# Kernel optimization log

Hardware: AMD Instinct MI355X
Metric: run time of the kernel (lower is better)

The kernel has to match this reference:

```python
import jax, jax.numpy as jnp
import numpy as np

NUM_HEADS = 8
NUM_GROUPS = 32
EPS = 1e-5


def group_norm(x, scale, bias):
    # x: (b, c, t)
    b, c, t = x.shape
    xg = x.reshape(b, NUM_GROUPS, c // NUM_GROUPS, t)
    mean = xg.mean(axis=(2, 3), keepdims=True)
    var = xg.var(axis=(2, 3), keepdims=True)
    xn = ((xg - mean) * jax.lax.rsqrt(var + EPS)).reshape(b, c, t)
    return xn * scale[None, :, None] + bias[None, :, None]


def setup_inputs() -> dict:
    key = jax.random.key(0)
    ks = jax.random.split(key, 3)
    b, c, h, w = 16, 512, 32, 32
    x = jax.random.normal(ks[0], (b, c, h, w), dtype=jnp.float32)
    gn_scale = jnp.ones((c,), jnp.float32)
    gn_bias = jnp.zeros((c,), jnp.float32)
    w_qkv = jax.random.normal(ks[1], (3 * c, c), jnp.float32) * (c ** -0.5)
    b_qkv = jnp.zeros((3 * c,), jnp.float32)
    w_proj = jax.random.normal(ks[2], (c, c), jnp.float32) * (c ** -0.5)
    b_proj = jnp.zeros((c,), jnp.float32)
    return {"x": x, "gn_scale": gn_scale, "gn_bias": gn_bias,
            "w_qkv": w_qkv, "b_qkv": b_qkv, "w_proj": w_proj, "b_proj": b_proj}


def reference(x, gn_scale, gn_bias, w_qkv, b_qkv, w_proj, b_proj):
    b, c, h, w = x.shape
    t = h * w
    xf = x.reshape(b, c, t)
    xn = group_norm(xf, gn_scale, gn_bias)
    # 1x1 conv1d == channel matmul: (b, 3c, t)
    qkv = jnp.einsum('oc,bct->bot', w_qkv, xn) + b_qkv[None, :, None]
    dh = c // NUM_HEADS
    qkv = qkv.reshape(b * NUM_HEADS, 3 * dh, t)
    q, k, v = jnp.split(qkv, 3, axis=1)  # each (b*H, dh, t)
    scale = dh ** -0.25
    logits = jnp.einsum('bct,bcs->bts', q * scale, k * scale)
    weight = jax.nn.softmax(logits.astype(jnp.float32), axis=-1).astype(logits.dtype)
    attn = jnp.einsum('bts,bcs->bct', weight, v)  # (b*H, dh, t)
    attn = attn.reshape(b, c, t)
    out = jnp.einsum('oc,bct->bot', w_proj, attn) + b_proj[None, :, None]
    return (xf + out).reshape(b, c, h, w)
```

## Files before the change

kernel.cpp:

```cpp
#include <hip/hip_runtime.h>
#include <hip/hip_bf16.h>

typedef __hip_bfloat16 bf16;
typedef __attribute__((ext_vector_type(8))) short short8;
typedef __attribute__((ext_vector_type(4))) short short4v;
typedef __attribute__((ext_vector_type(4))) float float4v;
typedef __attribute__((ext_vector_type(16))) float f32x16;
typedef __attribute__((ext_vector_type(4))) int int4v;

__device__ __forceinline__ float b2f(bf16 v) { return __bfloat162float(v); }
__device__ __forceinline__ bf16  f2b(float v) { return __float2bfloat16(v); }
__device__ __forceinline__ short f2s(float v) { bf16 h = f2b(v); return *reinterpret_cast<short*>(&h); }
__device__ __forceinline__ float s2f(short s) { bf16 h; *reinterpret_cast<short*>(&h) = s; return b2f(h); }
__device__ __forceinline__ short8 ld8(const bf16* p) { return *(const short8*)p; }

__device__ __forceinline__ float ldin(const void* p, size_t i, int f32) {
  return f32 ? ((const float*)p)[i] : b2f(((const bf16*)p)[i]);
}

__device__ __forceinline__ float4v mfma16(short8 a, short8 b, float4v c) {
  return __builtin_amdgcn_mfma_f32_16x16x32_bf16(a, b, c, 0, 0, 0);
}
__device__ __forceinline__ f32x16 mfma32(short8 a, short8 b, f32x16 c) {
  return __builtin_amdgcn_mfma_f32_32x32x16_bf16(a, b, c, 0, 0, 0);
}
__device__ __forceinline__ int cvtpk(float a, float b) {
  int r; asm("v_cvt_pk_bf16_f32 %0, %1, %2" : "=v"(r) : "v"(a), "v"(b)); return r;
}
__device__ __forceinline__ void plswap(int& x, int& y) {
  asm("v_permlane32_swap_b32 %0, %1" : "+v"(x), "+v"(y));
}

__device__ __forceinline__ void gload16(const void* g, void* l) {
  __builtin_amdgcn_global_load_lds((__attribute__((address_space(1))) void*)(void*)g,
                                   (__attribute__((address_space(3))) void*)l, 16, 0, 0);
}

#define K2SCALE 0.18033688011112042f
#define TSTRIDE 72

__global__ __launch_bounds__(256) void detect_kernel(const unsigned short* __restrict__ x,
                                                     int* __restrict__ flag) {
  __shared__ int h;
  if (threadIdx.x == 0) h = 0;
  __syncthreads();
  int local = 0;
  for (int i = threadIdx.x; i < 8192; i += 256)
    if ((x[i] & 0x7F80u) == 0x7F80u) local = 1;
  if (local) atomicOr(&h, 1);
  __syncthreads();
  if (threadIdx.x == 0) *flag = h;
}

__global__ __launch_bounds__(256) void pre_kernel(const void* __restrict__ s1, bf16* __restrict__ d1,
                                                  const void* __restrict__ s2, bf16* __restrict__ d2,
                                                  const void* __restrict__ s3, bf16* __restrict__ d3,
                                                  const void* __restrict__ s4, bf16* __restrict__ d4,
                                                  const void* __restrict__ x,
                                                  float2* __restrict__ stats,
                                                  const int* __restrict__ flagp) {
  const int f32 = *flagp;
  const int blk = blockIdx.x;
  const int tid = threadIdx.x;
  __shared__ float rs[4], rss[4];

  if (blk < 1027) {
    const void* src; bf16* dst; int base, n;
    if (blk < 768)       { src = s1; dst = d1; base = blk;        n = 786432; }
    else if (blk < 1024) { src = s2; dst = d2; base = blk - 768;  n = 262144; }
    else if (blk < 1026) { src = s3; dst = d3; base = blk - 1024; n = 1536;   }
    else                 { src = s4; dst = d4; base = 0;          n = 512;    }
    int i0 = (base * 256 + tid) * 4;
#pragma unroll
    for (int j = 0; j < 4; j++) {
      int i = i0 + j;
      if (i < n) dst[i] = f2b(ldin(src, i, f32));
    }
    return;
  }

  const int bg = blk - 1027;
  const int GSZ = 16 * 1024;
  const size_t base = (size_t)bg * GSZ;

  float s = 0.f, ss = 0.f;
  if (f32) {
    const float4v* xp = (const float4v*)((const float*)x + base) + tid;
#pragma unroll
    for (int i = 0; i < 16; i++) {
      float4v v = xp[i * 256];
#pragma unroll
      for (int j = 0; j < 4; j++) { s += v[j]; ss += v[j] * v[j]; }
    }
  } else {
    const short8* xp = (const short8*)((const bf16*)x + base) + tid;
#pragma unroll
    for (int i = 0; i < 8; i++) {
      short8 v = xp[i * 256];
#pragma unroll
      for (int j = 0; j < 8; j++) { float f = s2f(v[j]); s += f; ss += f * f; }
    }
  }
  for (int off = 32; off > 0; off >>= 1) {
    s  += __shfl_down(s, off);
    ss += __shfl_down(ss, off);
  }
  const int wave = tid >> 6, lane = tid & 63;
  if (lane == 0) { rs[wave] = s; rss[wave] = ss; }
  __syncthreads();
  if (tid == 0) {
    s  = rs[0] + rs[1] + rs[2] + rs[3];
    ss = rss[0] + rss[1] + rss[2] + rss[3];
    const float mean = s * (1.f / GSZ);
    const float var  = ss * (1.f / GSZ) - mean * mean;
    stats[bg] = make_float2(mean, rsqrtf(var + 1e-5f));
  }
}

__global__ __launch_bounds__(256) void gn_apply_kernel(const void* __restrict__ x,
                                                       const void* __restrict__ gsc,
                                                       const void* __restrict__ gbi,
                                                       const float2* __restrict__ stats,
                                                       bf16* __restrict__ xn,
                                                       const int* __restrict__ flagp) {
  const int f32 = *flagp;
  const int b = blockIdx.y;
  const int t0 = blockIdx.x * 64;
  const int cs = blockIdx.z * 128;
  const int tid = threadIdx.x;

  __shared__ float Aa[128], Bb[128];
  __shared__ short T[64][130];

  if (tid < 128) {
    const int c = cs + tid;
    const float2 st = stats[b * 32 + (c >> 4)];
    const float sc = ldin(gsc, c, f32), bi = ldin(gbi, c, f32);
    Aa[tid] = st.y * sc;
    Bb[tid] = bi - st.x * st.y * sc;
  }
  __syncthreads();

  const int row = tid >> 4;
  const int t4 = (tid & 15) * 4;
  if (f32) {
    const float* xb = (const float*)x + ((size_t)(b * 512 + cs)) * 1024 + t0 + t4;
#pragma unroll
    for (int st = 0; st < 8; st++) {
      const int c = row + st * 16;
      const float4v v = *(const float4v*)(xb + (size_t)c * 1024);
      const float aa = Aa[c], bb = Bb[c];
#pragma unroll
      for (int j = 0; j < 4; j++) T[t4 + j][c] = f2s(v[j] * aa + bb);
    }
  } else {
    const bf16* xb = (const bf16*)x + ((size_t)(b * 512 + cs)) * 1024 + t0 + t4;
#pragma unroll
    for (int st = 0; st < 8; st++) {
      const int c = row + st * 16;
      const short4v v = *(const short4v*)(xb + (size_t)c * 1024);
      const float aa = Aa[c], bb = Bb[c];
#pragma unroll
      for (int j = 0; j < 4; j++) T[t4 + j][c] = f2s(s2f(v[j]) * aa + bb);
    }
  }
  __syncthreads();

  const int cc = (tid & 63) * 2, tr = tid >> 6;
#pragma unroll
  for (int i = 0; i < 16; i++) {
    const int t2 = tr + i * 4;
    const int v = *(const int*)&T[t2][cc];
    *(int*)&xn[((size_t)(b * 1024 + t0 + t2)) * 512 + cs + cc] = v;
  }
}

__global__ __launch_bounds__(256) void qkv_kernel(const bf16* __restrict__ Wb,
                                                  const bf16* __restrict__ biasb,
                                                  const bf16* __restrict__ xn,
                                                  bf16* __restrict__ Qt,
                                                  bf16* __restrict__ Kt,
                                                  bf16* __restrict__ Vb) {
  const int bat = blockIdx.z;
  const int M0 = blockIdx.y * 128;
  const int N0 = blockIdx.x * 128;
  __shared__ short smem[18432];

  const int tid = threadIdx.x;
  const int w = tid >> 6, lane = tid & 63;
  const int col = lane & 15, g = lane >> 4;
  const int wm = (w & 1) * 64, wn = (w >> 1) * 64;

  float4v acc[4][4];
#pragma unroll
  for (int i = 0; i < 4; i++)
#pragma unroll
    for (int j = 0; j < 4; j++) acc[i][j] = (float4v)(0.f);

  int srco[2], dstb[2];
#pragma unroll
  for (int i = 0; i < 2; i++) {
    const int Gb = i * 256 + w * 64;
    dstb[i] = Gb * 8;
    const int G = Gb + lane;
    srco[i] = (G >> 2) * 512 + (G & 3) * 8;
  }
  const bf16* Ab  = Wb + (size_t)M0 * 512;
  const bf16* Bb2 = xn + ((size_t)bat * 1024 + N0) * 512;

#pragma unroll
  for (int i = 0; i < 2; i++) {
    gload16(Ab + srco[i],  &smem[dstb[i]]);
    gload16(Bb2 + srco[i], &smem[4096 + dstb[i]]);
  }
  __syncthreads();

  for (int it = 0; it < 16; ++it) {
    const int pb = it & 1;
    if (it < 15) {
      const int kn = it * 32 + 32;
      const int nb = (1 - pb) * 8192;
#pragma unroll
      for (int i = 0; i < 2; i++) {
        gload16(Ab + kn + srco[i],  &smem[nb + dstb[i]]);
        gload16(Bb2 + kn + srco[i], &smem[nb + 4096 + dstb[i]]);
      }
    }
    const short* Ap = &smem[pb * 8192];
    const short* Bp = Ap + 4096;
    short8 af[4], bf4[4];
#pragma unroll
    for (int mt = 0; mt < 4; mt++) af[mt] = *(const short8*)&Ap[(wm + mt * 16 + col) * 32 + g * 8];
#pragma unroll
    for (int nt = 0; nt < 4; nt++) bf4[nt] = *(const short8*)&Bp[(wn + nt * 16 + col) * 32 + g * 8];
#pragma unroll
    for (int mt = 0; mt < 4; mt++)
#pragma unroll
      for (int nt = 0; nt < 4; nt++) acc[mt][nt] = mfma16(af[mt], bf4[nt], acc[mt][nt]);
    __syncthreads();
  }

  const int sec = (M0 + wm) >> 6;
  const int h = sec / 3, kind = sec % 3;
  const size_t bh = (size_t)bat * 8 + h;
  const float qs = (kind == 0) ? K2SCALE : 1.f;
  short* Tw = smem + w * 4608;

  float bv[4][4];
#pragma unroll
  for (int mt = 0; mt < 4; mt++)
#pragma unroll
    for (int r = 0; r < 4; r++) bv[mt][r] = b2f(biasb[M0 + wm + mt * 16 + g * 4 + r]);

  if (kind == 2) {
#pragma unroll
    for (int mt = 0; mt < 4; mt++)
#pragma unroll
      for (int nt = 0; nt < 4; nt++)
#pragma unroll
        for (int r = 0; r < 4; r++) {
          const int lo = mt * 16 + g * 4 + r;
          const int lt = nt * 16 + col;
          Tw[lo * TSTRIDE + lt] = f2s(acc[mt][nt][r] + bv[mt][r]);
        }
#pragma unroll
    for (int j = 0; j < 8; j++) {
      const int lo = j * 8 + (lane >> 3);
      const int gr = lane & 7;
      short8 v = *(const short8*)&Tw[lo * TSTRIDE + gr * 8];
      *(short8*)(Vb + (bh * 64 + lo) * 1024 + N0 + wn + gr * 8) = v;
    }
  } else {
#pragma unroll
    for (int mt = 0; mt < 4; mt++)
#pragma unroll
      for (int nt = 0; nt < 4; nt++) {
        short4v pk;
#pragma unroll
        for (int r = 0; r < 4; r++) pk[r] = f2s((acc[mt][nt][r] + bv[mt][r]) * qs);
        *(short4v*)&Tw[(nt * 16 + col) * TSTRIDE + mt * 16 + g * 4] = pk;
      }
    bf16* dst = (kind == 0) ? Qt : Kt;
#pragma unroll
    for (int j = 0; j < 8; j++) {
      const int tl = j * 8 + (lane >> 3), c8 = (lane & 7) * 8;
      short8 v = *(const short8*)&Tw[tl * TSTRIDE + c8];
      *(short8*)(dst + (bh * 1024 + N0 + wn + tl) * 64 + c8) = v;
    }
  }
}

__global__ __launch_bounds__(256, 2) void attn_kernel(const bf16* __restrict__ Qt,
                                                      const bf16* __restrict__ Kt,
                                                      const bf16* __restrict__ Vb,
                                                      bf16* __restrict__ xattn) {
  const int bh = blockIdx.x;
  const int t0 = blockIdx.y * 256;
  const int b = bh >> 3, h = bh & 7;
  const int tid = threadIdx.x;
  const int w = tid >> 6, lane = tid & 63;
  const int qv = lane & 31, hh = lane >> 5;
  const int q0 = t0 + w * 64;

  __shared__ short Ks[8192];
  __shared__ short Vs[8192];

  const bf16* kbase = Kt + (size_t)bh * 65536;
  const bf16* vbase = Vb + (size_t)bh * 65536;

  int ksrc[2], vsrc[2];
  const int ldst0 = w * 1024, ldst1 = w * 1024 + 512;
#pragma unroll
  for (int i = 0; i < 2; i++) {
    const int G = w * 128 + i * 64 + lane;
    const int a = G >> 8, ks = (G >> 6) & 3, qvs = (G >> 1) & 31, hhs = G & 1;
    const int co = (ks * 2 + hhs) * 8;
    ksrc[i] = (a * 32 + qvs) * 64 + co;
    vsrc[i] = (a * 32 + qvs) * 1024 + co;
  }
  const int rb = (qv * 2 + hh) * 8;

  short8 qb[2][4];
#pragma unroll
  for (int qt = 0; qt < 2; qt++)
#pragma unroll
    for (int ks = 0; ks < 4; ks++)
      qb[qt][ks] = ld8(Qt + ((size_t)bh * 1024 + q0 + qt * 32 + qv) * 64 + ks * 16 + hh * 8);

  f32x16 O[2][2];
#pragma unroll
  for (int qt = 0; qt < 2; qt++)
#pragma unroll
    for (int o = 0; o < 2; o++) O[qt][o] = (f32x16)(0.f);
  float l[2] = {0.f, 0.f};
  short8 pa[2][4];

  gload16(kbase + ksrc[0], &Ks[ldst0]);
  gload16(kbase + ksrc[1], &Ks[ldst1]);
  gload16(vbase + vsrc[0], &Vs[ldst0]);
  gload16(vbase + vsrc[1], &Vs[ldst1]);
  __syncthreads();

#define SMAX(S, qt, a)                                                          \
  {                                                                             \
    _Pragma("unroll")                                                           \
    for (int j = 0; j < 16; j++) S[j] = __builtin_amdgcn_exp2f(S[j]);           \
    l[qt] += (((S[0] + S[1]) + (S[2] + S[3])) + ((S[4] + S[5]) + (S[6] + S[7])))\
       + (((S[8] + S[9]) + (S[10] + S[11])) + ((S[12] + S[13]) + (S[14] + S[15]))); \
    _Pragma("unroll")                                                           \
    for (int kp = 0; kp < 2; kp++) {                                            \
      int X  = cvtpk(S[8 * kp + 0], S[8 * kp + 1]);                             \
      int Y  = cvtpk(S[8 * kp + 4], S[8 * kp + 5]);                             \
      int X2 = cvtpk(S[8 * kp + 2], S[8 * kp + 3]);                             \
      int Y2 = cvtpk(S[8 * kp + 6], S[8 * kp + 7]);                             \
      plswap(X, Y);                                                             \
      plswap(X2, Y2);                                                           \
      const int4v wv = {X, X2, Y, Y2};                                          \
      pa[qt][(a) * 2 + kp] = __builtin_bit_cast(short8, wv);                    \
    }                                                                           \
  }

#pragma unroll 2
  for (int it = 0; it < 16; ++it) {
    const int cur = (it & 1) * 4096;
    const int nxt = 4096 - cur;
    if (it < 15) {
      gload16(kbase + (it + 1) * 4096 + ksrc[0], &Ks[nxt + ldst0]);
      gload16(kbase + (it + 1) * 4096 + ksrc[1], &Ks[nxt + ldst1]);
      gload16(vbase + (it + 1) * 64 + vsrc[0],   &Vs[nxt + ldst0]);
      gload16(vbase + (it + 1) * 64 + vsrc[1],   &Vs[nxt + ldst1]);
    }
#pragma unroll
    for (int a = 0; a < 2; a++) {
      short8 kf[4];
#pragma unroll
      for (int ks = 0; ks < 4; ks++)
        kf[ks] = *(const short8*)&Ks[cur + (a * 4 + ks) * 512 + rb];
#pragma unroll
      for (int qt = 0; qt < 2; qt++) {
        f32x16 S = (f32x16)(0.f);
#pragma unroll
        for (int ks = 0; ks < 4; ks++) S = mfma32(kf[ks], qb[qt][ks], S);
        SMAX(S, qt, a);
      }
    }
#pragma unroll
    for (int o = 0; o < 2; o++) {
      short8 vf[4];
#pragma unroll
      for (int ks = 0; ks < 4; ks++)
        vf[ks] = *(const short8*)&Vs[cur + (o * 4 + ks) * 512 + rb];
#pragma unroll
      for (int qt = 0; qt < 2; qt++)
#pragma unroll
        for (int ks = 0; ks < 4; ks++)
          O[qt][o] = mfma32(pa[qt][ks], vf[ks], O[qt][o]);
    }
    __syncthreads();
  }
#undef SMAX

#pragma unroll
  for (int qt = 0; qt < 2; qt++) {
    float lt = l[qt] + __shfl_xor(l[qt], 32);
    const float inv = 1.f / lt;
    float* lf = (float*)Ks + w * 64 + qt * 32;
    lf[qv] = inv;

    bf16* ob = xattn + ((size_t)b * 1024 + q0 + qt * 32 + 4 * hh) * 512 + h * 64 + qv;
#pragma unroll
    for (int r = 0; r < 16; r++) {
      const int qoff = (r & 3) + 8 * (r >> 2);
      const float iv = lf[qoff + 4 * hh];
      ob[(size_t)qoff * 512]      = f2b(O[qt][0][r] * iv);
      ob[(size_t)qoff * 512 + 32] = f2b(O[qt][1][r] * iv);
    }
  }
}

__global__ __launch_bounds__(256) void proj_kernel(const bf16* __restrict__ Wp,
                                                   const bf16* __restrict__ biasb,
                                                   const bf16* __restrict__ xattn,
                                                   const void* __restrict__ res,
                                                   void* __restrict__ out,
                                                   const int* __restrict__ flagp) {
  const int f32 = *flagp;
  const int bat = blockIdx.z;
  const int M0 = blockIdx.y * 128;
  const int N0 = blockIdx.x * 128;
  __shared__ short smem[18432];

  const int tid = threadIdx.x;
  const int w = tid >> 6, lane = tid & 63;
  const int col = lane & 15, g = lane >> 4;
  const int wm = (w & 1) * 64, wn = (w >> 1) * 64;

  float4v acc[4][4];
#pragma unroll
  for (int i = 0; i < 4; i++)
#pragma unroll
    for (int j = 0; j < 4; j++) acc[i][j] = (float4v)(0.f);

  int srco[2], dstb[2];
#pragma unroll
  for (int i = 0; i < 2; i++) {
    const int Gb = i * 256 + w * 64;
    dstb[i] = Gb * 8;
    const int G = Gb + lane;
    srco[i] = (G >> 2) * 512 + (G & 3) * 8;
  }
  const bf16* Ab  = Wp + (size_t)M0 * 512;
  const bf16* Bb2 = xattn + ((size_t)bat * 1024 + N0) * 512;

#pragma unroll
  for (int i = 0; i < 2; i++) {
    gload16(Ab + srco[i],  &smem[dstb[i]]);
    gload16(Bb2 + srco[i], &smem[4096 + dstb[i]]);
  }
  __syncthreads();

  for (int it = 0; it < 16; ++it) {
    const int pb = it & 1;
    if (it < 15) {
      const int kn = it * 32 + 32;
      const int nb = (1 - pb) * 8192;
#pragma unroll
      for (int i = 0; i < 2; i++) {
        gload16(Ab + kn + srco[i],  &smem[nb + dstb[i]]);
        gload16(Bb2 + kn + srco[i], &smem[nb + 4096 + dstb[i]]);
      }
    }
    const short* Ap = &smem[pb * 8192];
    const short* Bp = Ap + 4096;
    short8 af[4], bf4[4];
#pragma unroll
    for (int mt = 0; mt < 4; mt++) af[mt] = *(const short8*)&Ap[(wm + mt * 16 + col) * 32 + g * 8];
#pragma unroll
    for (int nt = 0; nt < 4; nt++) bf4[nt] = *(const short8*)&Bp[(wn + nt * 16 + col) * 32 + g * 8];
#pragma unroll
    for (int mt = 0; mt < 4; mt++)
#pragma unroll
      for (int nt = 0; nt < 4; nt++) acc[mt][nt] = mfma16(af[mt], bf4[nt], acc[mt][nt]);
    __syncthreads();
  }

  short* Tw = smem + w * 4608;
  float bv[4][4];
#pragma unroll
  for (int mt = 0; mt < 4; mt++)
#pragma unroll
    for (int r = 0; r < 4; r++) bv[mt][r] = b2f(biasb[M0 + wm + mt * 16 + g * 4 + r]);

#pragma unroll
  for (int mt = 0; mt < 4; mt++)
#pragma unroll
    for (int nt = 0; nt < 4; nt++)
#pragma unroll
      for (int r = 0; r < 4; r++) {
        const int lo = mt * 16 + g * 4 + r;
        const int lt = nt * 16 + col;
        Tw[lo * TSTRIDE + lt] = f2s(acc[mt][nt][r] + bv[mt][r]);
      }
#pragma unroll
  for (int j = 0; j < 8; j++) {
    const int lo = j * 8 + (lane >> 3);
    const int gr = lane & 7;
    short8 v = *(const short8*)&Tw[lo * TSTRIDE + gr * 8];
    const int o = M0 + wm + lo;
    const size_t ci = ((size_t)bat * 512 + o) * 1024 + N0 + wn + gr * 8;
    if (f32) {
      const float4v r0 = *(const float4v*)((const float*)res + ci);
      const float4v r1 = *(const float4v*)((const float*)res + ci + 4);
      float4v o0, o1;
#pragma unroll
      for (int e = 0; e < 4; e++) o0[e] = s2f(v[e]) + r0[e];
#pragma unroll
      for (int e = 0; e < 4; e++) o1[e] = s2f(v[e + 4]) + r1[e];
      *(float4v*)((float*)out + ci) = o0;
      *(float4v*)((float*)out + ci + 4) = o1;
    } else {
      const short8 rv = *(const short8*)((const bf16*)res + ci);
      short8 ov;
#pragma unroll
      for (int e = 0; e < 8; e++)
        ov[e] = f2s(s2f(v[e]) + s2f(rv[e]));
      *(short8*)((bf16*)out + ci) = ov;
    }
  }
}

extern "C" void kernel_launch(void* const* d_in, const int* in_sizes, int n_in,
                              void* d_out, int out_size, void* d_ws, size_t ws_size,
                              hipStream_t stream) {
  const void* x      = d_in[0];
  const void* gsc    = d_in[1];
  const void* gbi    = d_in[2];
  const void* w_qkv  = d_in[3];
  const void* b_qkv  = d_in[4];
  const void* w_proj = d_in[5];
  const void* b_proj = d_in[6];

  char* p = (char*)d_ws;
  int*    flag  = (int*)p;                 p += 256;
  float2* stats = (float2*)p;              p += 512 * sizeof(float2);
  bf16*   xn    = (bf16*)p;                p += (size_t)16 * 1024 * 512 * 2;
  bf16*   Qt    = (bf16*)p;                p += (size_t)128 * 1024 * 64 * 2;
  bf16*   Kt    = (bf16*)p;                p += (size_t)128 * 1024 * 64 * 2;
  bf16*   Vb    = (bf16*)p;                p += (size_t)128 * 64 * 1024 * 2;
  bf16*   Wqb   = (bf16*)p;                p += (size_t)1536 * 512 * 2;
  bf16*   Wpb   = (bf16*)p;                p += (size_t)512 * 512 * 2;
  bf16*   Bqb   = (bf16*)p;                p += (size_t)1536 * 2;
  bf16*   Bpb   = (bf16*)p;                p += (size_t)512 * 2;
  bf16*   xattn = (bf16*)p;

  detect_kernel<<<1, 256, 0, stream>>>((const unsigned short*)x, flag);
  pre_kernel<<<1539, 256, 0, stream>>>(w_qkv, Wqb, w_proj, Wpb,
                                       b_qkv, Bqb, b_proj, Bpb,
                                       x, stats, flag);
  gn_apply_kernel<<<dim3(16, 16, 4), 256, 0, stream>>>(x, gsc, gbi, stats, xn, flag);
  qkv_kernel<<<dim3(8, 12, 16), 256, 0, stream>>>(Wqb, Bqb, xn, Qt, Kt, Vb);
  attn_kernel<<<dim3(128, 4), 256, 0, stream>>>(Qt, Kt, Vb, xattn);
  proj_kernel<<<dim3(8, 4, 16), 256, 0, stream>>>(Wpb, Bpb, xattn, x, d_out, flag);
}
```

Measured before the change: 201.6 us.

## Widen QKV GEMM tile to 128x256 with 512-thread blocks

The QKV projection kernel now uses 8 waves per block covering a 128x256 output tile, so each weight tile loaded into shared memory is reused across twice as many token columns. Shared memory grows to hold the larger double-buffered B tile. The epilogue transposes through shared memory in two phases separated by barriers, because the staging area only fits four waves at a time. This cuts redundant weight loads, at the cost of fewer blocks, extra synchronisation in the epilogue and higher LDS use per block.

```diff
diff --git a/kernel.cpp b/kernel.cpp
--- a/kernel.cpp
+++ b/kernel.cpp
@@ -175,7 +175,7 @@
   }
 }
 
-__global__ __launch_bounds__(256) void qkv_kernel(const bf16* __restrict__ Wb,
+__global__ __launch_bounds__(512) void qkv_kernel(const bf16* __restrict__ Wb,
                                                   const bf16* __restrict__ biasb,
                                                   const bf16* __restrict__ xn,
                                                   bf16* __restrict__ Qt,
@@ -183,8 +183,8 @@
                                                   bf16* __restrict__ Vb) {
   const int bat = blockIdx.z;
   const int M0 = blockIdx.y * 128;
-  const int N0 = blockIdx.x * 128;
-  __shared__ short smem[18432];
+  const int N0 = blockIdx.x * 256;
+  __shared__ short smem[24576];
 
   const int tid = threadIdx.x;
   const int w = tid >> 6, lane = tid & 63;
@@ -197,36 +197,36 @@
 #pragma unroll
     for (int j = 0; j < 4; j++) acc[i][j] = (float4v)(0.f);
 
-  int srco[2], dstb[2];
+  const int GA = w * 64 + lane;
+  const int srcoA = (GA >> 2) * 512 + (GA & 3) * 8;
+  const int dstA  = w * 512;
+  int srcoB[2], dstB[2];
 #pragma unroll
   for (int i = 0; i < 2; i++) {
-    const int Gb = i * 256 + w * 64;
-    dstb[i] = Gb * 8;
-    const int G = Gb + lane;
-    srco[i] = (G >> 2) * 512 + (G & 3) * 8;
+    const int GB = w * 128 + i * 64 + lane;
+    srcoB[i] = (GB >> 2) * 512 + (GB & 3) * 8;
+    dstB[i]  = 4096 + (w * 128 + i * 64) * 8;
   }
   const bf16* Ab  = Wb + (size_t)M0 * 512;
   const bf16* Bb2 = xn + ((size_t)bat * 1024 + N0) * 512;
 
-#pragma unroll
-  for (int i = 0; i < 2; i++) {
-    gload16(Ab + srco[i],  &smem[dstb[i]]);
-    gload16(Bb2 + srco[i], &smem[4096 + dstb[i]]);
-  }
+  gload16(Ab + srcoA, &smem[dstA]);
+#pragma unroll
+  for (int i = 0; i < 2; i++)
+    gload16(Bb2 + srcoB[i], &smem[dstB[i]]);
   __syncthreads();
 
   for (int it = 0; it < 16; ++it) {
     const int pb = it & 1;
     if (it < 15) {
       const int kn = it * 32 + 32;
-      const int nb = (1 - pb) * 8192;
-#pragma unroll
-      for (int i = 0; i < 2; i++) {
-        gload16(Ab + kn + srco[i],  &smem[nb + dstb[i]]);
-        gload16(Bb2 + kn + srco[i], &smem[nb + 4096 + dstb[i]]);
-      }
-    }
-    const short* Ap = &smem[pb * 8192];
+      const int nb = (1 - pb) * 12288;
+      gload16(Ab + kn + srcoA, &smem[nb + dstA]);
+#pragma unroll
+      for (int i = 0; i < 2; i++)
+        gload16(Bb2 + kn + srcoB[i], &smem[nb + dstB[i]]);
+    }
+    const short* Ap = &smem[pb * 12288];
     const short* Bp = Ap + 4096;
     short8 af[4], bf4[4];
 #pragma unroll
@@ -244,7 +244,6 @@
   const int h = sec / 3, kind = sec % 3;
   const size_t bh = (size_t)bat * 8 + h;
   const float qs = (kind == 0) ? K2SCALE : 1.f;
-  short* Tw = smem + w * 4608;
 
   float bv[4][4];
 #pragma unroll
@@ -252,41 +251,48 @@
 #pragma unroll
     for (int r = 0; r < 4; r++) bv[mt][r] = b2f(biasb[M0 + wm + mt * 16 + g * 4 + r]);
 
-  if (kind == 2) {
-#pragma unroll
-    for (int mt = 0; mt < 4; mt++)
-#pragma unroll
-      for (int nt = 0; nt < 4; nt++)
-#pragma unroll
-        for (int r = 0; r < 4; r++) {
-          const int lo = mt * 16 + g * 4 + r;
-          const int lt = nt * 16 + col;
-          Tw[lo * TSTRIDE + lt] = f2s(acc[mt][nt][r] + bv[mt][r]);
+#pragma unroll
+  for (int ph = 0; ph < 2; ph++) {
+    if ((w >> 2) == ph) {
+      short* Tw = smem + (w & 3) * 4608;
+      if (kind == 2) {
+#pragma unroll
+        for (int mt = 0; mt < 4; mt++)
+#pragma unroll
+          for (int nt = 0; nt < 4; nt++)
+#pragma unroll
+            for (int r = 0; r < 4; r++) {
+              const int lo = mt * 16 + g * 4 + r;
+              const int lt = nt * 16 + col;
+              Tw[lo * TSTRIDE + lt] = f2s(acc[mt][nt][r] + bv[mt][r]);
+            }
+#pragma unroll
+        for (int j = 0; j < 8; j++) {
+          const int lo = j * 8 + (lane >> 3);
+          const int gr = lane & 7;
+          short8 v = *(const short8*)&Tw[lo * TSTRIDE + gr * 8];
+          *(short8*)(Vb + (bh * 64 + lo) * 1024 + N0 + wn + gr * 8) = v;
         }
-#pragma unroll
-    for (int j = 0; j < 8; j++) {
-      const int lo = j * 8 + (lane >> 3);
-      const int gr = lane & 7;
-      short8 v = *(const short8*)&Tw[lo * TSTRIDE + gr * 8];
-      *(short8*)(Vb + (bh * 64 + lo) * 1024 + N0 + wn + gr * 8) = v;
-    }
-  } else {
-#pragma unroll
-    for (int mt = 0; mt < 4; mt++)
-#pragma unroll
-      for (int nt = 0; nt < 4; nt++) {
-        short4v pk;
-#pragma unroll
-        for (int r = 0; r < 4; r++) pk[r] = f2s((acc[mt][nt][r] + bv[mt][r]) * qs);
-        *(short4v*)&Tw[(nt * 16 + col) * TSTRIDE + mt * 16 + g * 4] = pk;
+      } else {
+#pragma unroll
+        for (int mt = 0; mt < 4; mt++)
+#pragma unroll
+          for (int nt = 0; nt < 4; nt++) {
+            short4v pk;
+#pragma unroll
+            for (int r = 0; r < 4; r++) pk[r] = f2s((acc[mt][nt][r] + bv[mt][r]) * qs);
+            *(short4v*)&Tw[(nt * 16 + col) * TSTRIDE + mt * 16 + g * 4] = pk;
+          }
+        bf16* dst = (kind == 0) ? Qt : Kt;
+#pragma unroll
+        for (int j = 0; j < 8; j++) {
+          const int tl = j * 8 + (lane >> 3), c8 = (lane & 7) * 8;
+          short8 v = *(const short8*)&Tw[tl * TSTRIDE + c8];
+          *(short8*)(dst + (bh * 1024 + N0 + wn + tl) * 64 + c8) = v;
+        }
       }
-    bf16* dst = (kind == 0) ? Qt : Kt;
-#pragma unroll
-    for (int j = 0; j < 8; j++) {
-      const int tl = j * 8 + (lane >> 3), c8 = (lane & 7) * 8;
-      short8 v = *(const short8*)&Tw[tl * TSTRIDE + c8];
-      *(short8*)(dst + (bh * 1024 + N0 + wn + tl) * 64 + c8) = v;
-    }
+    }
+    __syncthreads();
   }
 }
 
@@ -558,7 +564,7 @@
                                        b_qkv, Bqb, b_proj, Bpb,
                                        x, stats, flag);
   gn_apply_kernel<<<dim3(16, 16, 4), 256, 0, stream>>>(x, gsc, gbi, stats, xn, flag);
-  qkv_kernel<<<dim3(8, 12, 16), 256, 0, stream>>>(Wqb, Bqb, xn, Qt, Kt, Vb);
+  qkv_kernel<<<dim3(4, 12, 16), 512, 0, stream>>>(Wqb, Bqb, xn, Qt, Kt, Vb);
   attn_kernel<<<dim3(128, 4), 256, 0, stream>>>(Qt, Kt, Vb, xattn);
   proj_kernel<<<dim3(8, 4, 16), 256, 0, stream>>>(Wpb, Bpb, xattn, x, d_out, flag);
 }
```

Result: no change. 203.8 us (+1.1%).
